# Kernel tuning notes

Hardware: AMD Instinct MI355X
Metric: run time of the kernel (lower is better)

The kernel has to match this reference:

```python
import jax, jax.numpy as jnp
import numpy as np

NUM_LOW, NUM_HIGH, DIM = 8192, 1024, 2048
EPS = 1e-10


def sparsemax(z):
    # z: [..., K]; Martins & Astudillo sparsemax along last axis.
    K = z.shape[-1]
    z_sorted = jnp.flip(jnp.sort(z, axis=-1), axis=-1)          # descending
    z_cum = jnp.cumsum(z_sorted, axis=-1)
    k = jnp.arange(1, K + 1, dtype=z.dtype)
    support = (1.0 + k * z_sorted) > z_cum                       # bool [..., K]
    k_sup = jnp.sum(support, axis=-1, keepdims=True)             # int [..., 1]
    tau = (jnp.take_along_axis(z_cum, k_sup - 1, axis=-1) - 1.0) / k_sup.astype(z.dtype)
    return jnp.maximum(z - tau, 0.0)


def normalize_rows(x, eps=EPS):
    return x / (jnp.sum(x, axis=1, keepdims=True) + eps)


def setup_inputs() -> dict:
    key = jax.random.key(0)
    k1, k2, k3, k4 = jax.random.split(key, 4)

    def xavier(k, shape):
        bound = float(np.sqrt(6.0 / (shape[0] + shape[1])))
        return jax.random.uniform(k, shape, jnp.float32, -bound, bound)

    return {
        "low_w": xavier(k1, (NUM_LOW, DIM)),    # low Concepts parameter
        "high_w": xavier(k2, (NUM_HIGH, DIM)),  # high Concepts parameter
        "Wq": xavier(k3, (DIM, DIM)),           # q_linear.weight (keep_head_dim, n_head=1)
        "Wk": xavier(k4, (DIM, DIM)),           # k_linear.weight
        "norm_low_concepts": 1,
        "norm_high_concepts": 1,
    }


def reference(low_w, high_w, Wq, Wk, norm_low_concepts, norm_high_concepts):
    # Concepts modules: return (possibly normalized) concepts + cosine similarity.
    low_normed = low_w / jnp.linalg.norm(low_w, axis=1, keepdims=True)
    low_concepts = low_normed if norm_low_concepts else low_w
    low_cos = low_normed @ low_normed.T                          # [NL, NL]

    high_normed = high_w / jnp.linalg.norm(high_w, axis=1, keepdims=True)
    high_concepts = high_normed if norm_high_concepts else high_w
    high_cos = high_normed @ high_normed.T                       # [NH, NH]

    # detach_low_concepts=True -> queries do not receive gradients
    low_q = jax.lax.stop_gradient(low_concepts)

    # ModifiedMultiHeadAttention (n_head=1, keep_head_dim -> d_head=DIM; eval mode,
    # so smooth_max is identity and sparsemax is deterministic).
    q = low_q @ Wq.T                                             # [NL, D]
    k = high_concepts @ Wk.T                                     # [NH, D]
    scale = 1.0 / jnp.sqrt(jnp.asarray(DIM, q.dtype))
    attn = sparsemax((q @ k.T) * scale)                          # [NL, NH]
    high_related_low = attn @ high_concepts                      # [NL, D]

    # output_high_concepts_type == "high_plus_low": add back aggregated low concepts
    aggregated_low = normalize_rows(attn.T) @ low_q              # [NH, D]
    output_high_concepts = high_related_low + attn @ aggregated_low  # [NL, D]

    return (low_concepts, low_cos, output_high_concepts, high_cos, attn)
```

## Files before the change

### kernel.cpp

```cpp
#include <hip/hip_runtime.h>
#include <hip/hip_bf16.h>
#include <stdint.h>

#define NL   8192
#define NHI  1024
#define DIMV 2048

typedef __attribute__((ext_vector_type(8))) short short8;
typedef __attribute__((ext_vector_type(4))) float f32x4;

__device__ __forceinline__ unsigned short f2bf(float x){
  unsigned u = __float_as_uint(x);
  u += 0x7FFFu + ((u >> 16) & 1u);
  return (unsigned short)(u >> 16);
}
__device__ __forceinline__ float bf2f(unsigned short b){
  return __uint_as_float(((unsigned)b) << 16);
}
__device__ __forceinline__ unsigned pack2bf(float a, float b){
  return (unsigned)f2bf(a) | ((unsigned)f2bf(b) << 16);
}

__device__ __forceinline__ void gload16(const void* g, void* l){
  __builtin_amdgcn_global_load_lds(
      (const __attribute__((address_space(1))) unsigned int*)g,
      (__attribute__((address_space(3))) unsigned int*)l, 16, 0, 0);
}

__global__ __launch_bounds__(256)
void prep_kernel(const float* __restrict__ low_w, const float* __restrict__ high_w,
                 const float* __restrict__ Wq, const float* __restrict__ Wk,
                 float* __restrict__ out_lowc, unsigned short* __restrict__ lowN,
                 unsigned short* __restrict__ highN,
                 unsigned short* __restrict__ WqT, unsigned short* __restrict__ WkT){
  __shared__ __align__(16) char smem[8448];
  int id = blockIdx.x;
  if(id < 9216){
    const float* W; float* oF; unsigned short* oB; int row;
    if(id < 8192){ W = low_w; oF = out_lowc; oB = lowN; row = id; }
    else         { W = high_w; oF = nullptr; oB = highN; row = id - 8192; }
    const float* r = W + (size_t)row * DIMV;
    int base = threadIdx.x * 8;
    float4 x0 = *(const float4*)(r + base);
    float4 x1 = *(const float4*)(r + base + 4);
    float ss = x0.x*x0.x + x0.y*x0.y + x0.z*x0.z + x0.w*x0.w
             + x1.x*x1.x + x1.y*x1.y + x1.z*x1.z + x1.w*x1.w;
    #pragma unroll
    for(int s = 1; s < 64; s <<= 1) ss += __shfl_xor(ss, s, 64);
    float* red = (float*)smem;
    if((threadIdx.x & 63) == 0) red[threadIdx.x >> 6] = ss;
    __syncthreads();
    float tot = red[0] + red[1] + red[2] + red[3];
    float inv = 1.0f / sqrtf(tot);
    float y0=x0.x*inv, y1=x0.y*inv, y2=x0.z*inv, y3=x0.w*inv;
    float y4=x1.x*inv, y5=x1.y*inv, y6=x1.z*inv, y7=x1.w*inv;
    if(oF){
      float* o = oF + (size_t)row * DIMV + base;
      *(float4*)o       = make_float4(y0,y1,y2,y3);
      *(float4*)(o + 4) = make_float4(y4,y5,y6,y7);
    }
    uint4 u;
    u.x = pack2bf(y0,y1); u.y = pack2bf(y2,y3);
    u.z = pack2bf(y4,y5); u.w = pack2bf(y6,y7);
    *(uint4*)(oB + (size_t)row * DIMV + base) = u;
  } else {
    id -= 9216;
    const float* in; unsigned short* outp;
    if(id < 1024){ in = Wq; outp = WqT; } else { in = Wk; outp = WkT; id -= 1024; }
    unsigned short (*tile)[65] = (unsigned short(*)[65])smem;
    int tx = id & 31, ty = id >> 5;
    int c0 = tx * 64, r0 = ty * 64;
    int t = threadIdx.x;
    int ci = t & 63, r4 = t >> 6;
    #pragma unroll
    for(int k = 0; k < 16; k++){
      int r = k * 4 + r4;
      tile[r][ci] = f2bf(in[(size_t)(r0 + r) * 2048 + c0 + ci]);
    }
    __syncthreads();
    #pragma unroll
    for(int k = 0; k < 16; k++){
      int cc = k * 4 + r4;
      outp[(size_t)(c0 + cc) * 2048 + r0 + ci] = tile[ci][cc];
    }
  }
}

template<int OUT_BF16, int MIRROR>
__global__ __launch_bounds__(256, 2)
void gemm_bt_kernel(const unsigned short* __restrict__ A,
                    const unsigned short* __restrict__ Bt,
                    float* __restrict__ Cf, unsigned short* __restrict__ Cb,
                    int M, int N, int K, float scale){
  __shared__ __align__(16) char smem[32768];
  unsigned short* sA = (unsigned short*)smem;
  unsigned short* sB = sA + 128 * 64;

  int tid = threadIdx.x, lane = tid & 63, wid = tid >> 6;
  int mBase, nBase;
  if(MIRROR){
    int orig = blockIdx.x;
    int id = (orig & 7) * 260 + (orig >> 3);
    int Si = 0, rem = id;
    for(;;){ int rl = 10 + 16*(15 - Si); if(rem < rl) break; rem -= rl; Si++; }
    int bi, bj;
    if(rem < 10){
      int ti = 0;
      while((ti+1)*4 - (((ti+1)*ti) >> 1) <= rem) ti++;
      int off = ti*4 - ((ti*(ti-1)) >> 1);
      int tj = ti + (rem - off);
      bi = Si*4 + ti; bj = Si*4 + tj;
    } else {
      int r2 = rem - 10;
      int Sj = Si + 1 + (r2 >> 4);
      int t = r2 & 15;
      bi = Si*4 + (t >> 2); bj = Sj*4 + (t & 3);
    }
    mBase = bi * 128; nBase = bj * 128;
  } else {
    int gx = gridDim.x, gy = gridDim.y;
    int nwg = gx * gy;
    int id = blockIdx.y * gx + blockIdx.x;
    if((nwg & 7) == 0){ int cpx = nwg >> 3; id = (id & 7) * cpx + (id >> 3); }
    mBase = (id / gx) * 128; nBase = (id % gx) * 128;
  }

  int chRow = lane >> 3;
  int chCol = (lane & 7) * 8;
  int wm = wid >> 1, wn = wid & 1;

  f32x4 acc[4][4];
  #pragma unroll
  for(int i=0;i<4;i++)
    #pragma unroll
    for(int j=0;j<4;j++) acc[i][j] = (f32x4){0.f,0.f,0.f,0.f};

  int kChunk = K / (int)gridDim.z;
  int kStart = kChunk * (int)blockIdx.z;
  if(!OUT_BF16) Cf += (size_t)blockIdx.z * M * N;

  for(int k0 = kStart; k0 < kStart + kChunk; k0 += 64){
    #pragma unroll
    for(int i = 0; i < 4; i++){
      int ch = wid * 4 + i;
      int arow = ch * 8 + chRow;
      gload16(A  + (size_t)(mBase + arow) * K + k0 + chCol, &sA[ch * 512]);
      gload16(Bt + (size_t)(nBase + arow) * K + k0 + chCol, &sB[ch * 512]);
    }
    __syncthreads();
    #pragma unroll
    for(int kk = 0; kk < 64; kk += 32){
      short8 a[4], b[4];
      int krd = kk + (lane >> 4) * 8;
      #pragma unroll
      for(int i = 0; i < 4; i++){
        int row = wm * 64 + i * 16 + (lane & 15);
        a[i] = *reinterpret_cast<const short8*>(&sA[row * 64 + krd]);
        int col = wn * 64 + i * 16 + (lane & 15);
        b[i] = *reinterpret_cast<const short8*>(&sB[col * 64 + krd]);
      }
      #pragma unroll
      for(int i = 0; i < 4; i++)
        #pragma unroll
        for(int j = 0; j < 4; j++)
          acc[i][j] = __builtin_amdgcn_mfma_f32_16x16x32_bf16(a[i], b[j], acc[i][j], 0, 0, 0);
    }
    __syncthreads();
  }

  #pragma unroll
  for(int i = 0; i < 4; i++){
    #pragma unroll
    for(int j = 0; j < 4; j++){
      int row = mBase + wm * 64 + i * 16 + (lane >> 4) * 4;
      int col = nBase + wn * 64 + j * 16 + (lane & 15);
      #pragma unroll
      for(int r = 0; r < 4; r++){
        float v = acc[i][j][r] * scale;
        size_t off = (size_t)(row + r) * N + col;
        if(OUT_BF16) Cb[off] = f2bf(v);
        else         Cf[off] = v;
      }
    }
  }

  if(MIRROR && mBase != nBase){
    float* tf = (float*)smem;
    #pragma unroll
    for(int rq = 0; rq < 4; rq++){
      int qm = rq >> 1, qn = rq & 1;
      __syncthreads();
      if(wm == qm && wn == qn){
        #pragma unroll
        for(int i = 0; i < 4; i++)
          #pragma unroll
          for(int j = 0; j < 4; j++){
            int rl = i * 16 + (lane >> 4) * 4;
            int cl = j * 16 + (lane & 15);
            #pragma unroll
            for(int r = 0; r < 4; r++)
              tf[(rl + r) * 65 + cl] = acc[i][j][r] * scale;
          }
      }
      __syncthreads();
      int mr = tid >> 2, seg = tid & 3;
      size_t obase = (size_t)(nBase + qn * 64 + mr) * N + mBase + qm * 64 + seg * 16;
      #pragma unroll
      for(int k4 = 0; k4 < 4; k4++){
        float4 v;
        v.x = tf[(seg * 16 + k4 * 4 + 0) * 65 + mr];
        v.y = tf[(seg * 16 + k4 * 4 + 1) * 65 + mr];
        v.z = tf[(seg * 16 + k4 * 4 + 2) * 65 + mr];
        v.w = tf[(seg * 16 + k4 * 4 + 3) * 65 + mr];
        *(float4*)(Cf + obase + k4 * 4) = v;
      }
    }
  }
}

__global__ __launch_bounds__(256)
void sparsemax_kernel(float* __restrict__ S, unsigned short* __restrict__ attnBf,
                      const float* __restrict__ hcPart, float* __restrict__ out_highcos){
  int bid = blockIdx.x;
  if(bid >= 2048){
    size_t i = ((size_t)(bid - 2048) * 256 + threadIdx.x) * 8;
    float4 a0 = *(const float4*)(hcPart + i);
    float4 a1 = *(const float4*)(hcPart + i + 4);
    float4 b0 = *(const float4*)(hcPart + 1048576 + i);
    float4 b1 = *(const float4*)(hcPart + 1048576 + i + 4);
    *(float4*)(out_highcos + i)     = make_float4(a0.x+b0.x, a0.y+b0.y, a0.z+b0.z, a0.w+b0.w);
    *(float4*)(out_highcos + i + 4) = make_float4(a1.x+b1.x, a1.y+b1.y, a1.z+b1.z, a1.w+b1.w);
    return;
  }
  int wid = threadIdx.x >> 6, lane = threadIdx.x & 63;
  int row = bid * 4 + wid;
  float* z = S + (size_t)row * NHI;
  float v[16];
  #pragma unroll
  for(int j = 0; j < 16; j++) v[j] = z[j * 64 + lane];
  float mx = v[0];
  #pragma unroll
  for(int j = 1; j < 16; j++) mx = fmaxf(mx, v[j]);
  #pragma unroll
  for(int s = 1; s < 64; s <<= 1) mx = fmaxf(mx, __shfl_xor(mx, s, 64));
  float lo = mx - 1.0f, hi = mx;
  for(int it = 0; it < 40; it++){
    float mid = 0.5f * (lo + hi);
    float sum = 0.f;
    #pragma unroll
    for(int j = 0; j < 16; j++) sum += fmaxf(v[j] - mid, 0.f);
    #pragma unroll
    for(int s = 1; s < 64; s <<= 1) sum += __shfl_xor(sum, s, 64);
    if(sum >= 1.0f) lo = mid; else hi = mid;
  }
  float cnt = 0.f, ssum = 0.f;
  #pragma unroll
  for(int j = 0; j < 16; j++){
    if(v[j] > lo){ cnt += 1.f; ssum += v[j]; }
  }
  #pragma unroll
  for(int s = 1; s < 64; s <<= 1){
    cnt  += __shfl_xor(cnt,  s, 64);
    ssum += __shfl_xor(ssum, s, 64);
  }
  float tau = (ssum - 1.0f) / cnt;
  #pragma unroll
  for(int j = 0; j < 16; j++){
    float a = fmaxf(v[j] - tau, 0.f);
    z[j * 64 + lane] = a;
    attnBf[(size_t)row * NHI + j * 64 + lane] = f2bf(a);
  }
}

__global__ __launch_bounds__(256)
void colsum_part_kernel(const float* __restrict__ attn, float* __restrict__ part){
  int chunk = blockIdx.x;
  int t = threadIdx.x;
  const float* p = attn + (size_t)chunk * 32 * NHI;
  float a0=0,a1=0,a2=0,a3=0;
  for(int r = 0; r < 32; r++){
    a0 += p[(size_t)r*NHI + t];
    a1 += p[(size_t)r*NHI + t + 256];
    a2 += p[(size_t)r*NHI + t + 512];
    a3 += p[(size_t)r*NHI + t + 768];
  }
  float* q = part + (size_t)chunk * NHI;
  q[t]=a0; q[t+256]=a1; q[t+512]=a2; q[t+768]=a3;
}

__global__ __launch_bounds__(256)
void transpose3_kernel(const unsigned short* __restrict__ attnB, unsigned short* __restrict__ attnT,
                       const unsigned short* __restrict__ lowN,  unsigned short* __restrict__ lowNT,
                       const unsigned short* __restrict__ highN, unsigned short* __restrict__ highNT,
                       const float* __restrict__ part, float* __restrict__ colsum){
  int id = blockIdx.x;
  if(id >= 6656){
    int c = (id - 6656) * 256 + threadIdx.x;
    float s = 0.f;
    for(int i = 0; i < 256; i++) s += part[(size_t)i * NHI + c];
    colsum[c] = s;
    return;
  }
  __shared__ unsigned short tile[64][65];
  const unsigned short* in; unsigned short* out; int R, C, tx, ty;
  if(id < 2048){        in = attnB; out = attnT;  R = NL;  C = NHI;  tx = id & 15; ty = id >> 4; }
  else if(id < 6144){ id -= 2048;
                        in = lowN;  out = lowNT;  R = NL;  C = DIMV; tx = id & 31; ty = id >> 5; }
  else {              id -= 6144;
                        in = highN; out = highNT; R = NHI; C = DIMV; tx = id & 31; ty = id >> 5; }
  int c0 = tx * 64, r0 = ty * 64;
  int t = threadIdx.x;
  int ci = t & 63, r4 = t >> 6;
  #pragma unroll
  for(int k = 0; k < 16; k++){
    int r = k * 4 + r4;
    tile[r][ci] = in[(size_t)(r0 + r) * C + c0 + ci];
  }
  __syncthreads();
  #pragma unroll
  for(int k = 0; k < 16; k++){
    int cc = k * 4 + r4;
    out[(size_t)(c0 + cc) * R + r0 + ci] = tile[ci][cc];
  }
}

__global__ __launch_bounds__(256)
void mt_kernel(const unsigned short* __restrict__ highNT, const float* __restrict__ aggP,
               const float* __restrict__ colsum, unsigned short* __restrict__ Mt){
  int idx = blockIdx.x * 256 + threadIdx.x;
  int h = idx & 1023;
  float s = aggP[idx] + aggP[idx + 2097152];
  float val = bf2f(highNT[idx]) + s / (colsum[h] + 1e-10f);
  Mt[idx] = f2bf(val);
}

extern "C" void kernel_launch(void* const* d_in, const int* in_sizes, int n_in,
                              void* d_out, int out_size, void* d_ws, size_t ws_size,
                              hipStream_t stream){
  const float* low_w  = (const float*)d_in[0];
  const float* high_w = (const float*)d_in[1];
  const float* Wq     = (const float*)d_in[2];
  const float* Wk     = (const float*)d_in[3];
  float* out = (float*)d_out;

  char* ws = (char*)d_ws;
  unsigned short* lowN  = (unsigned short*)(ws);
  float*          aggP  = (float*)(ws);
  unsigned short* highN = (unsigned short*)(ws + 33554432);
  unsigned short* WqT   = (unsigned short*)(ws + 37748736);
  unsigned short* WkT   = (unsigned short*)(ws + 46137344);
  unsigned short* attnB = (unsigned short*)(ws + 37748736);
  unsigned short* G     = (unsigned short*)(ws + 54525952);
  unsigned short* R2t   = (unsigned short*)(ws + 62914560);
  unsigned short* lowNT = (unsigned short*)(ws + 54525952);
  float*          part  = (float*)(ws + 88080384);
  float*          colsum= (float*)(ws + 88080384 + 1048576);
  unsigned short* attnT = (unsigned short*)(ws + 92274688);
  float*          hcPart= (float*)(ws + 109051904);
  unsigned short* Mt    = (unsigned short*)(ws + 109051904);
  unsigned short* highNT= (unsigned short*)(ws + 113246208);

  float* out_lowc    = out;
  float* out_lowcos  = out + 16777216;
  float* out_high    = out + 83886080;
  float* out_highcos = out + 100663296;
  float* out_attn    = out + 101711872;

  const float scl = 1.0f / sqrtf((float)DIMV);

  prep_kernel<<<11264, 256, 0, stream>>>(low_w, high_w, Wq, Wk,
                                         out_lowc, lowN, highN, WqT, WkT);
  gemm_bt_kernel<0,1><<<2080, 256, 0, stream>>>(lowN, lowN, out_lowcos, nullptr,
                                                NL, NL, DIMV, 1.0f);
  gemm_bt_kernel<1,0><<<dim3(16,16), 256, 0, stream>>>(WqT, WkT, nullptr, G,
                                                       DIMV, DIMV, DIMV, 1.0f);
  gemm_bt_kernel<0,0><<<dim3(8,8,2), 256, 0, stream>>>(highN, highN, hcPart, nullptr,
                                                       NHI, NHI, DIMV, 1.0f);
  gemm_bt_kernel<1,0><<<dim3(16,8), 256, 0, stream>>>(highN, G, nullptr, R2t,
                                                      NHI, DIMV, DIMV, 1.0f);
  gemm_bt_kernel<0,0><<<dim3(8,64), 256, 0, stream>>>(lowN, R2t, out_attn, nullptr,
                                                      NL, NHI, DIMV, scl);
  sparsemax_kernel<<<2560, 256, 0, stream>>>(out_attn, attnB, hcPart, out_highcos);
  colsum_part_kernel<<<256, 256, 0, stream>>>(out_attn, part);
  transpose3_kernel<<<6660, 256, 0, stream>>>(attnB, attnT, lowN, lowNT, highN, highNT,
                                              part, colsum);
  gemm_bt_kernel<0,0><<<dim3(8,16,2), 256, 0, stream>>>(lowNT, attnT, aggP, nullptr,
                                                        DIMV, NHI, NL, 1.0f);
  mt_kernel<<<8192, 256, 0, stream>>>(highNT, aggP, colsum, Mt);
  gemm_bt_kernel<0,0><<<dim3(16,64), 256, 0, stream>>>(attnB, Mt, out_high, nullptr,
                                                       NL, DIMV, NHI, 1.0f);
}
```

Baseline: 601.6 us.

## Merge independent GEMM launches and reductions into combined multi-role kernels

The symmetric low-cos GEMM, the WqT·WkT GEMM and the split-K high-cos GEMM now run as one grid that dispatches by block index to a shared inlined GEMM core. The column-sum partial reduction moves into the transpose kernel, and the final column-sum reduction moves into the aggregation GEMM launch. This removes several kernel launches and the gaps between them, and lets small GEMMs fill the tail of the large one. The cost is runtime flags instead of template constants in the GEMM core, which may affect register use or code generation.

```diff
diff --git a/kernel.cpp b/kernel.cpp
--- a/kernel.cpp
+++ b/kernel.cpp
@@ -86,45 +86,14 @@
   }
 }
 
-template<int OUT_BF16, int MIRROR>
-__global__ __launch_bounds__(256, 2)
-void gemm_bt_kernel(const unsigned short* __restrict__ A,
-                    const unsigned short* __restrict__ Bt,
-                    float* __restrict__ Cf, unsigned short* __restrict__ Cb,
-                    int M, int N, int K, float scale){
-  __shared__ __align__(16) char smem[32768];
+__device__ __forceinline__ void gemm_core(
+    const unsigned short* __restrict__ A, const unsigned short* __restrict__ Bt,
+    float* __restrict__ Cf, unsigned short* __restrict__ Cb,
+    int M, int N, int K, float scale, int mBase, int nBase,
+    int kStart, int kChunk, int outBf16, int mirror, char* smem){
   unsigned short* sA = (unsigned short*)smem;
   unsigned short* sB = sA + 128 * 64;
-
   int tid = threadIdx.x, lane = tid & 63, wid = tid >> 6;
-  int mBase, nBase;
-  if(MIRROR){
-    int orig = blockIdx.x;
-    int id = (orig & 7) * 260 + (orig >> 3);
-    int Si = 0, rem = id;
-    for(;;){ int rl = 10 + 16*(15 - Si); if(rem < rl) break; rem -= rl; Si++; }
-    int bi, bj;
-    if(rem < 10){
-      int ti = 0;
-      while((ti+1)*4 - (((ti+1)*ti) >> 1) <= rem) ti++;
-      int off = ti*4 - ((ti*(ti-1)) >> 1);
-      int tj = ti + (rem - off);
-      bi = Si*4 + ti; bj = Si*4 + tj;
-    } else {
-      int r2 = rem - 10;
-      int Sj = Si + 1 + (r2 >> 4);
-      int t = r2 & 15;
-      bi = Si*4 + (t >> 2); bj = Sj*4 + (t & 3);
-    }
-    mBase = bi * 128; nBase = bj * 128;
-  } else {
-    int gx = gridDim.x, gy = gridDim.y;
-    int nwg = gx * gy;
-    int id = blockIdx.y * gx + blockIdx.x;
-    if((nwg & 7) == 0){ int cpx = nwg >> 3; id = (id & 7) * cpx + (id >> 3); }
-    mBase = (id / gx) * 128; nBase = (id % gx) * 128;
-  }
-
   int chRow = lane >> 3;
   int chCol = (lane & 7) * 8;
   int wm = wid >> 1, wn = wid & 1;
@@ -134,10 +103,6 @@
   for(int i=0;i<4;i++)
     #pragma unroll
     for(int j=0;j<4;j++) acc[i][j] = (f32x4){0.f,0.f,0.f,0.f};
-
-  int kChunk = K / (int)gridDim.z;
-  int kStart = kChunk * (int)blockIdx.z;
-  if(!OUT_BF16) Cf += (size_t)blockIdx.z * M * N;
 
   for(int k0 = kStart; k0 < kStart + kChunk; k0 += 64){
     #pragma unroll
@@ -178,13 +143,13 @@
       for(int r = 0; r < 4; r++){
         float v = acc[i][j][r] * scale;
         size_t off = (size_t)(row + r) * N + col;
-        if(OUT_BF16) Cb[off] = f2bf(v);
-        else         Cf[off] = v;
+        if(outBf16) Cb[off] = f2bf(v);
+        else        Cf[off] = v;
       }
     }
   }
 
-  if(MIRROR && mBase != nBase){
+  if(mirror && mBase != nBase){
     float* tf = (float*)smem;
     #pragma unroll
     for(int rq = 0; rq < 4; rq++){
@@ -218,6 +183,83 @@
   }
 }
 
+template<int OUT_BF16>
+__global__ __launch_bounds__(256, 2)
+void gemm_bt_kernel(const unsigned short* __restrict__ A,
+                    const unsigned short* __restrict__ Bt,
+                    float* __restrict__ Cf, unsigned short* __restrict__ Cb,
+                    int M, int N, int K, float scale){
+  __shared__ __align__(16) char smem[32768];
+  int gx = gridDim.x, gy = gridDim.y;
+  int nwg = gx * gy;
+  int id = blockIdx.y * gx + blockIdx.x;
+  if((nwg & 7) == 0){ int cpx = nwg >> 3; id = (id & 7) * cpx + (id >> 3); }
+  int mBase = (id / gx) * 128, nBase = (id % gx) * 128;
+  int kChunk = K / (int)gridDim.z;
+  int kStart = kChunk * (int)blockIdx.z;
+  if(!OUT_BF16) Cf += (size_t)blockIdx.z * M * N;
+  gemm_core(A, Bt, Cf, Cb, M, N, K, scale, mBase, nBase, kStart, kChunk, OUT_BF16, 0, smem);
+}
+
+__global__ __launch_bounds__(256, 2)
+void mega1_kernel(const unsigned short* __restrict__ lowN, float* __restrict__ out_lowcos,
+                  const unsigned short* __restrict__ WqT, const unsigned short* __restrict__ WkT,
+                  unsigned short* __restrict__ G,
+                  const unsigned short* __restrict__ highN, float* __restrict__ hcPart){
+  __shared__ __align__(16) char smem[32768];
+  int bid = blockIdx.x;
+  if(bid < 2080){
+    int id = (bid & 7) * 260 + (bid >> 3);
+    int Si = 0, rem = id;
+    for(;;){ int rl = 10 + 16*(15 - Si); if(rem < rl) break; rem -= rl; Si++; }
+    int bi, bj;
+    if(rem < 10){
+      int ti = 0;
+      while((ti+1)*4 - (((ti+1)*ti) >> 1) <= rem) ti++;
+      int off = ti*4 - ((ti*(ti-1)) >> 1);
+      int tj = ti + (rem - off);
+      bi = Si*4 + ti; bj = Si*4 + tj;
+    } else {
+      int r2 = rem - 10;
+      int Sj = Si + 1 + (r2 >> 4);
+      int t = r2 & 15;
+      bi = Si*4 + (t >> 2); bj = Sj*4 + (t & 3);
+    }
+    gemm_core(lowN, lowN, out_lowcos, nullptr, NL, NL, DIMV, 1.0f,
+              bi*128, bj*128, 0, DIMV, 0, 1, smem);
+  } else if(bid < 2336){
+    int id2 = bid - 2080;
+    int s = (id2 & 7) * 32 + (id2 >> 3);
+    gemm_core(WqT, WkT, nullptr, G, DIMV, DIMV, DIMV, 1.0f,
+              (s >> 4)*128, (s & 15)*128, 0, DIMV, 1, 0, smem);
+  } else {
+    int id3 = bid - 2336;
+    int z = id3 >> 6, w = id3 & 63;
+    int s = (w & 7) * 8 + (w >> 3);
+    gemm_core(highN, highN, hcPart + (size_t)z * 1048576, nullptr, NHI, NHI, DIMV, 1.0f,
+              (s >> 3)*128, (s & 7)*128, z*1024, 1024, 0, 0, smem);
+  }
+}
+
+__global__ __launch_bounds__(256, 2)
+void megaagg_kernel(const unsigned short* __restrict__ lowNT,
+                    const unsigned short* __restrict__ attnT, float* __restrict__ aggP,
+                    const float* __restrict__ part, float* __restrict__ colsum){
+  __shared__ __align__(16) char smem[32768];
+  int bid = blockIdx.x;
+  if(bid < 256){
+    int z = bid >> 7, w = bid & 127;
+    int s = (w & 7) * 16 + (w >> 3);
+    gemm_core(lowNT, attnT, aggP + (size_t)z * 2097152, nullptr, DIMV, NHI, NL, 1.0f,
+              (s >> 3)*128, (s & 7)*128, z*4096, 4096, 0, 0, smem);
+  } else {
+    int c = (bid - 256) * 256 + threadIdx.x;
+    float s = 0.f;
+    for(int i = 0; i < 256; i++) s += part[(size_t)i * NHI + c];
+    colsum[c] = s;
+  }
+}
+
 __global__ __launch_bounds__(256)
 void sparsemax_kernel(float* __restrict__ S, unsigned short* __restrict__ attnBf,
                       const float* __restrict__ hcPart, float* __restrict__ out_highcos){
@@ -273,32 +315,24 @@
 }
 
 __global__ __launch_bounds__(256)
-void colsum_part_kernel(const float* __restrict__ attn, float* __restrict__ part){
-  int chunk = blockIdx.x;
-  int t = threadIdx.x;
-  const float* p = attn + (size_t)chunk * 32 * NHI;
-  float a0=0,a1=0,a2=0,a3=0;
-  for(int r = 0; r < 32; r++){
-    a0 += p[(size_t)r*NHI + t];
-    a1 += p[(size_t)r*NHI + t + 256];
-    a2 += p[(size_t)r*NHI + t + 512];
-    a3 += p[(size_t)r*NHI + t + 768];
-  }
-  float* q = part + (size_t)chunk * NHI;
-  q[t]=a0; q[t+256]=a1; q[t+512]=a2; q[t+768]=a3;
-}
-
-__global__ __launch_bounds__(256)
 void transpose3_kernel(const unsigned short* __restrict__ attnB, unsigned short* __restrict__ attnT,
                        const unsigned short* __restrict__ lowN,  unsigned short* __restrict__ lowNT,
                        const unsigned short* __restrict__ highN, unsigned short* __restrict__ highNT,
-                       const float* __restrict__ part, float* __restrict__ colsum){
+                       const float* __restrict__ attnF, float* __restrict__ part){
   int id = blockIdx.x;
   if(id >= 6656){
-    int c = (id - 6656) * 256 + threadIdx.x;
-    float s = 0.f;
-    for(int i = 0; i < 256; i++) s += part[(size_t)i * NHI + c];
-    colsum[c] = s;
+    int chunk = id - 6656;
+    int t = threadIdx.x;
+    const float* p = attnF + (size_t)chunk * 32 * NHI;
+    float a0=0,a1=0,a2=0,a3=0;
+    for(int r = 0; r < 32; r++){
+      a0 += p[(size_t)r*NHI + t];
+      a1 += p[(size_t)r*NHI + t + 256];
+      a2 += p[(size_t)r*NHI + t + 512];
+      a3 += p[(size_t)r*NHI + t + 768];
+    }
+    float* q = part + (size_t)chunk * NHI;
+    q[t]=a0; q[t+256]=a1; q[t+512]=a2; q[t+768]=a3;
     return;
   }
   __shared__ unsigned short tile[64][65];
@@ -370,23 +404,16 @@
 
   prep_kernel<<<11264, 256, 0, stream>>>(low_w, high_w, Wq, Wk,
                                          out_lowc, lowN, highN, WqT, WkT);
-  gemm_bt_kernel<0,1><<<2080, 256, 0, stream>>>(lowN, lowN, out_lowcos, nullptr,
-                                                NL, NL, DIMV, 1.0f);
-  gemm_bt_kernel<1,0><<<dim3(16,16), 256, 0, stream>>>(WqT, WkT, nullptr, G,
-                                                       DIMV, DIMV, DIMV, 1.0f);
-  gemm_bt_kernel<0,0><<<dim3(8,8,2), 256, 0, stream>>>(highN, highN, hcPart, nullptr,
-                                                       NHI, NHI, DIMV, 1.0f);
-  gemm_bt_kernel<1,0><<<dim3(16,8), 256, 0, stream>>>(highN, G, nullptr, R2t,
-                                                      NHI, DIMV, DIMV, 1.0f);
-  gemm_bt_kernel<0,0><<<dim3(8,64), 256, 0, stream>>>(lowN, R2t, out_attn, nullptr,
-                                                      NL, NHI, DIMV, scl);
+  mega1_kernel<<<2464, 256, 0, stream>>>(lowN, out_lowcos, WqT, WkT, G, highN, hcPart);
+  gemm_bt_kernel<1><<<dim3(16,8), 256, 0, stream>>>(highN, G, nullptr, R2t,
+                                                    NHI, DIMV, DIMV, 1.0f);
+  gemm_bt_kernel<0><<<dim3(8,64), 256, 0, stream>>>(lowN, R2t, out_attn, nullptr,
+                                                    NL, NHI, DIMV, scl);
   sparsemax_kernel<<<2560, 256, 0, stream>>>(out_attn, attnB, hcPart, out_highcos);
-  colsum_part_kernel<<<256, 256, 0, stream>>>(out_attn, part);
-  transpose3_kernel<<<6660, 256, 0, stream>>>(attnB, attnT, lowN, lowNT, highN, highNT,
-                                              part, colsum);
-  gemm_bt_kernel<0,0><<<dim3(8,16,2), 256, 0, stream>>>(lowNT, attnT, aggP, nullptr,
-                                                        DIMV, NHI, NL, 1.0f);
+  transpose3_kernel<<<6912, 256, 0, stream>>>(attnB, attnT, lowN, lowNT, highN, highNT,
+                                              out_attn, part);
+  megaagg_kernel<<<260, 256, 0, stream>>>(lowNT, attnT, aggP, part, colsum);
   mt_kernel<<<8192, 256, 0, stream>>>(highNT, aggP, colsum, Mt);
-  gemm_bt_kernel<0,0><<<dim3(16,64), 256, 0, stream>>>(attnB, Mt, out_high, nullptr,
-                                                       NL, DIMV, NHI, 1.0f);
-}
+  gemm_bt_kernel<0><<<dim3(16,64), 256, 0, stream>>>(attnB, Mt, out_high, nullptr,
+                                                     NL, DIMV, NHI, 1.0f);
+}
```

Result: faster. 546.7 us (-9.1%).
